# Kernel optimization log

Measured on AMD Instinct MI355X. Metric: run time of the kernel, lower is better.

The kernel has to match this reference:

```python
import jax, jax.numpy as jnp
import numpy as np

B, H, W, E = 4, 128, 128, 512
NH = 16
WH = WW = 8
DFF = 2048
EPS = 1e-5
N = WH * WW  # tokens per window
HD = E // NH  # head dim

# static relative-position index table: bias[q, k] = table[k_h - q_h + WH-1, k_w - q_w + WW-1]
_coords = np.stack(np.meshgrid(np.arange(WH), np.arange(WW), indexing='ij'), -1).reshape(-1, 2)  # (N, 2)
_rel = _coords[None, :, :] - _coords[:, None, :]  # (N, N, 2), key - query
_IDX_H = _rel[..., 0] + WH - 1
_IDX_W = _rel[..., 1] + WW - 1


def setup_inputs() -> dict:
    key = jax.random.key(0)
    ks = jax.random.split(key, 8)
    s = 0.02
    return {
        'x': jax.random.normal(ks[0], (B, H * W, E), jnp.float32),
        'in_proj_weight': jax.random.normal(ks[1], (3 * E, E), jnp.float32) * s,
        'in_proj_bias': jnp.zeros((3 * E,), jnp.float32),
        'out_proj_weight': jax.random.normal(ks[2], (E, E), jnp.float32) * s,
        'out_proj_bias': jnp.zeros((E,), jnp.float32),
        'pos_emb': jax.random.normal(ks[3], (2 * WH - 1, 2 * WW - 1, 1), jnp.float32) * s,
        'lin1_w': jax.random.normal(ks[4], (DFF, E), jnp.float32) * s,
        'lin1_b': jnp.zeros((DFF,), jnp.float32),
        'lin2_w': jax.random.normal(ks[5], (E, DFF), jnp.float32) * s,
        'lin2_b': jnp.zeros((E,), jnp.float32),
        'ln1_w': jnp.ones((E,), jnp.float32),
        'ln1_b': jnp.zeros((E,), jnp.float32),
        'ln2_w': jnp.ones((E,), jnp.float32),
        'ln2_b': jnp.zeros((E,), jnp.float32),
    }


def _layer_norm(y, g, b):
    m = y.mean(-1, keepdims=True)
    v = y.var(-1, keepdims=True)
    return (y - m) * jax.lax.rsqrt(v + EPS) * g + b


def _forward(x, in_proj_weight, in_proj_bias, out_proj_weight, out_proj_bias,
             pos_emb, lin1_w, lin1_b, lin2_w, lin2_b, ln1_w, ln1_b, ln2_w, ln2_b):
    # relative positional bias shared across heads: (1, N, N)
    bias = pos_emb[_IDX_H, _IDX_W, :].transpose(2, 0, 1)

    def attn(y):
        # window partition: (B, H*W, E) -> (B*nWin, N, E)
        yw = y.reshape(B, H // WH, WH, W // WW, WW, E)
        yw = yw.transpose(0, 1, 3, 2, 4, 5).reshape(-1, N, E)
        qw, kw, vw = jnp.split(in_proj_weight, 3, axis=0)
        qb, kb, vb = jnp.split(in_proj_bias, 3, axis=0)
        q = (yw @ qw.T + qb).reshape(-1, N, NH, HD).transpose(0, 2, 1, 3)  # (Bw, h, N, d)
        k = (yw @ kw.T + kb).reshape(-1, N, NH, HD).transpose(0, 2, 1, 3)
        v = (yw @ vw.T + vb).reshape(-1, N, NH, HD).transpose(0, 2, 1, 3)
        scores = jnp.einsum('bhqd,bhkd->bhqk', q, k) / np.sqrt(HD).astype(np.float32)
        scores = scores + bias[None]  # broadcast over windows and heads
        a = jax.nn.softmax(scores, axis=-1)
        o = jnp.einsum('bhqk,bhkd->bhqd', a, v)
        o = o.transpose(0, 2, 1, 3).reshape(-1, N, E)
        o = o @ out_proj_weight.T + out_proj_bias
        # reverse window partition
        o = o.reshape(B, H // WH, W // WW, WH, WW, E)
        return o.transpose(0, 1, 3, 2, 4, 5).reshape(B, H * W, E)

    # post-norm (norm_first=False): x = norm1(x + SA(x)); x = norm2(x + FF(x))
    z = _layer_norm(x + attn(x), ln1_w, ln1_b)
    ff = jax.nn.relu(z @ lin1_w.T + lin1_b) @ lin2_w.T + lin2_b
    return _layer_norm(z + ff, ln2_w, ln2_b)


def reference(x, in_proj_weight, in_proj_bias, out_proj_weight, out_proj_bias,
              pos_emb, lin1_w, lin1_b, lin2_w, lin2_b, ln1_w, ln1_b, ln2_w, ln2_b):
    return _forward(x, in_proj_weight, in_proj_bias, out_proj_weight, out_proj_bias,
                    pos_emb, lin1_w, lin1_b, lin2_w, lin2_b, ln1_w, ln1_b, ln2_w, ln2_b)
```

## Files before the change

### kernel.cpp

```cpp
#include <hip/hip_runtime.h>
#include <hip/hip_bf16.h>

#define NTOK   65536
#define E_     512
#define NH_    16
#define HD_    32
#define DFF_   2048
#define N3E    1536

typedef __attribute__((ext_vector_type(8))) short short8;
typedef __attribute__((ext_vector_type(4))) short short4t;
typedef __attribute__((ext_vector_type(4))) float floatx4;

__device__ inline float b2f(short u) {
    union { float f; unsigned int i; } x;
    x.i = ((unsigned int)(unsigned short)u) << 16;
    return x.f;
}
__device__ inline short f2bs(float f) {
    __hip_bfloat16 h = __float2bfloat16(f);
    return *reinterpret_cast<short*>(&h);
}

__global__ __launch_bounds__(256) void cvt_kernel(const float* __restrict__ in,
                                                  __hip_bfloat16* __restrict__ out, int n) {
    int i = (blockIdx.x * 256 + threadIdx.x) * 8;
    if (i >= n) return;
    if (i + 7 < n) {
        float4 a = *(const float4*)(in + i);
        float4 b = *(const float4*)(in + i + 4);
        short8 o;
        o[0] = f2bs(a.x); o[1] = f2bs(a.y); o[2] = f2bs(a.z); o[3] = f2bs(a.w);
        o[4] = f2bs(b.x); o[5] = f2bs(b.y); o[6] = f2bs(b.z); o[7] = f2bs(b.w);
        *(short8*)(out + i) = o;
    } else {
        for (int u = i; u < n; ++u) out[u] = __float2bfloat16(in[u]);
    }
}

template<int EPI>
__global__ __launch_bounds__(512) void gemm2_kernel(
    const __hip_bfloat16* __restrict__ A,
    const __hip_bfloat16* __restrict__ Bw,
    const float* __restrict__ bias,
    const void* __restrict__ res,
    void* __restrict__ out,
    int M, int N, int K)
{
    __shared__ __align__(16) short As[2][128 * 64];
    __shared__ __align__(16) short Bs[2][256 * 64];

    const int tid  = threadIdx.x;
    const int wid  = tid >> 6;
    const int lane = tid & 63;
    const int tileN = blockIdx.x * 256;
    const int tileM = blockIdx.y * 128;

    const int wm = (wid >> 2) * 64;
    const int wn = (wid & 3) * 64;
    const int lm = lane & 15;
    const int g  = lane >> 4;

    const int lr = lane >> 3;
    const int ss = (lane & 7) ^ lr;

    const __hip_bfloat16* gA = A  + (size_t)(tileM + wid * 16 + lr) * K + ss * 8;
    const __hip_bfloat16* gB = Bw + (size_t)(tileN + wid * 32 + lr) * K + ss * 8;

    floatx4 acc[4][4];
    #pragma unroll
    for (int i = 0; i < 4; ++i)
        #pragma unroll
        for (int j = 0; j < 4; ++j)
            acc[i][j] = (floatx4){0.f, 0.f, 0.f, 0.f};

#define STAGE2(b, k0)                                                                     \
    {                                                                                     \
        _Pragma("unroll")                                                                 \
        for (int q = 0; q < 2; ++q)                                                       \
            __builtin_amdgcn_global_load_lds(                                             \
                (const __attribute__((address_space(1))) void*)(gA + (size_t)(q * 8) * K + (k0)), \
                (__attribute__((address_space(3))) void*)(&As[b][(wid * 2 + q) * 512]),   \
                16, 0, 0);                                                                \
        _Pragma("unroll")                                                                 \
        for (int q = 0; q < 4; ++q)                                                       \
            __builtin_amdgcn_global_load_lds(                                             \
                (const __attribute__((address_space(1))) void*)(gB + (size_t)(q * 8) * K + (k0)), \
                (__attribute__((address_space(3))) void*)(&Bs[b][(wid * 4 + q) * 512]),   \
                16, 0, 0);                                                                \
    }

    const int NT = K >> 6;

    STAGE2(0, 0)
    STAGE2(1, 64)
    asm volatile("s_waitcnt vmcnt(6)\ns_barrier" ::: "memory");

    const int lsw = (lm & 7);

    for (int t = 0; t < NT; ++t) {
        const int b = t & 1;
        const short* pa = As[b];
        const short* pb = Bs[b];

        #pragma unroll
        for (int ks = 0; ks < 2; ++ks) {
            short8 af[4], bfr[4];
            const int cs = ks * 4 + g;
            const int so = (cs ^ lsw) * 8;
            #pragma unroll
            for (int i = 0; i < 4; ++i)
                af[i] = *(const short8*)(pa + (wm + i * 16 + lm) * 64 + so);
            #pragma unroll
            for (int j = 0; j < 4; ++j)
                bfr[j] = *(const short8*)(pb + (wn + j * 16 + lm) * 64 + so);

            __builtin_amdgcn_s_setprio(1);
            #pragma unroll
            for (int i = 0; i < 4; ++i)
                #pragma unroll
                for (int j = 0; j < 4; ++j)
                    acc[i][j] = __builtin_amdgcn_mfma_f32_16x16x32_bf16(af[i], bfr[j], acc[i][j], 0, 0, 0);
            __builtin_amdgcn_s_setprio(0);
        }

        if (t + 1 < NT) {
            asm volatile("s_waitcnt lgkmcnt(0)\ns_barrier" ::: "memory");
            if (t + 2 < NT) {
                STAGE2(b, (t + 2) * 64)
                asm volatile("s_waitcnt vmcnt(6)\ns_barrier" ::: "memory");
            } else {
                asm volatile("s_waitcnt vmcnt(0)\ns_barrier" ::: "memory");
            }
        }
    }
#undef STAGE2

    const int rbase = g * 4;
    #pragma unroll
    for (int i = 0; i < 4; ++i) {
        const int rl = wm + i * 16 + rbase;
        #pragma unroll
        for (int j = 0; j < 4; ++j) {
            const int n = tileN + wn + j * 16 + lm;
            const float bv = bias[n];
            #pragma unroll
            for (int r = 0; r < 4; ++r) {
                const int m = tileM + rl + r;
                const size_t idx = (size_t)m * N + n;
                float v = acc[i][j][r] + bv;
                if (EPI == 0) {
                    ((__hip_bfloat16*)out)[idx] = __float2bfloat16(v);
                } else if (EPI == 1) {
                    v += ((const float*)res)[idx];
                    ((float*)out)[idx] = v;
                } else if (EPI == 2) {
                    v = v > 0.f ? v : 0.f;
                    ((__hip_bfloat16*)out)[idx] = __float2bfloat16(v);
                } else {
                    v += __bfloat162float(((const __hip_bfloat16*)res)[idx]);
                    ((float*)out)[idx] = v;
                }
            }
        }
    }
}

__global__ __launch_bounds__(64) void attn_kernel(
    const __hip_bfloat16* __restrict__ qkv,
    const float* __restrict__ pos,
    __hip_bfloat16* __restrict__ obuf)
{
    __shared__ __align__(16) short vt[32][72];
    __shared__ __align__(16) short pl[64][72];
    __shared__ float ps[232];

    const int bwin = blockIdx.x;
    const int win  = bwin & 255;
    const int bat  = bwin >> 8;
    const int h    = blockIdx.y;
    const int l    = threadIdx.x;
    const int l15  = l & 15;
    const int g    = l >> 4;
    const int g8   = g * 8;

    const int base0 = bat * 16384 + (win >> 4) * 1024 + (win & 15) * 8;

    for (int u = l; u < 225; u += 64) ps[u] = pos[u];

    const int tok_l = base0 + (l >> 3) * 128 + (l & 7);
    const short8* vp = (const short8*)(qkv + (size_t)tok_l * N3E + 1024 + h * HD_);
    #pragma unroll
    for (int u = 0; u < 4; ++u) {
        short8 vv = vp[u];
        #pragma unroll
        for (int e = 0; e < 8; ++e) vt[u * 8 + e][l] = vv[e];
    }

    const int tokbase = base0 + (l15 >> 3) * 128 + (l15 & 7);
    short8 qf[4], kf[4];
    #pragma unroll
    for (int j = 0; j < 4; ++j) {
        const size_t tb = (size_t)(tokbase + 256 * j) * N3E + h * HD_ + g8;
        qf[j] = *(const short8*)(qkv + tb);
        kf[j] = *(const short8*)(qkv + tb + 512);
    }
    __syncthreads();

    floatx4 st[4][4];
    #pragma unroll
    for (int i = 0; i < 4; ++i)
        #pragma unroll
        for (int j = 0; j < 4; ++j)
            st[i][j] = __builtin_amdgcn_mfma_f32_16x16x32_bf16(
                kf[i], qf[j], (floatx4){0.f, 0.f, 0.f, 0.f}, 0, 0, 0);

    const float scale = 0.17677669529663687f;
    int kb[4];
    #pragma unroll
    for (int r = 0; r < 4; ++r) {
        const int qq = g * 4 + r;
        kb[r] = (qq >> 3) * 15 + (qq & 7);
    }

    #pragma unroll
    for (int j = 0; j < 4; ++j) {
        const int q   = j * 16 + l15;
        const int qoi = 112 - (q >> 3) * 15 - (q & 7);
        float p[16];
        float mx = -1e30f;
        #pragma unroll
        for (int i = 0; i < 4; ++i)
            #pragma unroll
            for (int r = 0; r < 4; ++r) {
                const float sv = st[i][j][r] * scale + ps[30 * i + kb[r] + qoi];
                p[i * 4 + r] = sv;
                mx = fmaxf(mx, sv);
            }
        mx = fmaxf(mx, __shfl_xor(mx, 16));
        mx = fmaxf(mx, __shfl_xor(mx, 32));
        float sum = 0.f;
        #pragma unroll
        for (int u = 0; u < 16; ++u) { p[u] = __expf(p[u] - mx); sum += p[u]; }
        sum += __shfl_xor(sum, 16);
        sum += __shfl_xor(sum, 32);
        const float inv = 1.f / sum;
        #pragma unroll
        for (int i = 0; i < 4; ++i) {
            short4t pk;
            #pragma unroll
            for (int r = 0; r < 4; ++r) pk[r] = f2bs(p[i * 4 + r] * inv);
            *(short4t*)&pl[q][i * 16 + g * 4] = pk;
        }
    }
    __syncthreads();

    short8 vb[2][2];
    #pragma unroll
    for (int nt = 0; nt < 2; ++nt)
        #pragma unroll
        for (int kk = 0; kk < 2; ++kk)
            vb[nt][kk] = *(const short8*)&vt[nt * 16 + l15][kk * 32 + g8];

    floatx4 o[4][2];
    #pragma unroll
    for (int j = 0; j < 4; ++j)
        #pragma unroll
        for (int nt = 0; nt < 2; ++nt)
            o[j][nt] = (floatx4){0.f, 0.f, 0.f, 0.f};

    #pragma unroll
    for (int j = 0; j < 4; ++j) {
        #pragma unroll
        for (int kk = 0; kk < 2; ++kk) {
            const short8 pa = *(const short8*)&pl[j * 16 + l15][kk * 32 + g8];
            #pragma unroll
            for (int nt = 0; nt < 2; ++nt)
                o[j][nt] = __builtin_amdgcn_mfma_f32_16x16x32_bf16(
                    pa, vb[nt][kk], o[j][nt], 0, 0, 0);
        }
    }

    #pragma unroll
    for (int r = 0; r < 4; ++r) {
        const int qq = g * 4 + r;
        const int tb = base0 + (qq >> 3) * 128 + (qq & 7);
        #pragma unroll
        for (int j = 0; j < 4; ++j) {
            __hip_bfloat16* op = obuf + (size_t)(tb + 256 * j) * E_ + h * HD_ + l15;
            op[0]  = __float2bfloat16(o[j][0][r]);
            op[16] = __float2bfloat16(o[j][1][r]);
        }
    }
}

template<int OUTMODE>
__global__ __launch_bounds__(256) void ln_kernel(
    const float* __restrict__ in, const float* __restrict__ gw,
    const float* __restrict__ gb, void* __restrict__ out)
{
    const int row  = blockIdx.x * 4 + (threadIdx.x >> 6);
    const int lane = threadIdx.x & 63;
    const float* rp = in + (size_t)row * 512 + lane * 8;
    float4 v0 = *(const float4*)rp;
    float4 v1 = *(const float4*)(rp + 4);
    float s  = v0.x + v0.y + v0.z + v0.w + v1.x + v1.y + v1.z + v1.w;
    float sq = v0.x * v0.x + v0.y * v0.y + v0.z * v0.z + v0.w * v0.w
             + v1.x * v1.x + v1.y * v1.y + v1.z * v1.z + v1.w * v1.w;
    #pragma unroll
    for (int off = 32; off > 0; off >>= 1) {
        s  += __shfl_xor(s, off);
        sq += __shfl_xor(sq, off);
    }
    const float mean = s * (1.f / 512.f);
    const float var  = sq * (1.f / 512.f) - mean * mean;
    const float rstd = rsqrtf(var + 1e-5f);
    const int c = lane * 8;
    float4 g0 = *(const float4*)(gw + c), g1 = *(const float4*)(gw + c + 4);
    float4 b0 = *(const float4*)(gb + c), b1 = *(const float4*)(gb + c + 4);
    float r[8];
    r[0] = (v0.x - mean) * rstd * g0.x + b0.x;
    r[1] = (v0.y - mean) * rstd * g0.y + b0.y;
    r[2] = (v0.z - mean) * rstd * g0.z + b0.z;
    r[3] = (v0.w - mean) * rstd * g0.w + b0.w;
    r[4] = (v1.x - mean) * rstd * g1.x + b1.x;
    r[5] = (v1.y - mean) * rstd * g1.y + b1.y;
    r[6] = (v1.z - mean) * rstd * g1.z + b1.z;
    r[7] = (v1.w - mean) * rstd * g1.w + b1.w;
    if (OUTMODE == 0) {
        short8 o;
        #pragma unroll
        for (int e = 0; e < 8; ++e) o[e] = f2bs(r[e]);
        *(short8*)((__hip_bfloat16*)out + (size_t)row * 512 + c) = o;
    } else {
        float* po = (float*)out + (size_t)row * 512 + c;
        *(float4*)po       = make_float4(r[0], r[1], r[2], r[3]);
        *(float4*)(po + 4) = make_float4(r[4], r[5], r[6], r[7]);
    }
}

static const size_t OFF_WQKV = 0;
static const size_t OFF_WOUT = 1572864;
static const size_t OFF_W1   = 2097152;
static const size_t OFF_W2   = 4194304;
static const size_t OFF_XB   = 6291456;
static const size_t OFF_ZB   = 73400320;
static const size_t OFF_QKVC = 140509184;
static const size_t OFF_OBUFC= 341835776;
static const size_t OFF_H1C  = OFF_QKVC;

extern "C" void kernel_launch(void* const* d_in, const int* in_sizes, int n_in,
                              void* d_out, int out_size, void* d_ws, size_t ws_size,
                              hipStream_t stream) {
    (void)in_sizes; (void)n_in; (void)out_size; (void)ws_size;
    const float* x    = (const float*)d_in[0];
    const float* wqkv = (const float*)d_in[1];
    const float* bqkv = (const float*)d_in[2];
    const float* wout = (const float*)d_in[3];
    const float* bout = (const float*)d_in[4];
    const float* pos  = (const float*)d_in[5];
    const float* w1   = (const float*)d_in[6];
    const float* b1   = (const float*)d_in[7];
    const float* w2   = (const float*)d_in[8];
    const float* b2   = (const float*)d_in[9];
    const float* g1   = (const float*)d_in[10];
    const float* bb1  = (const float*)d_in[11];
    const float* g2   = (const float*)d_in[12];
    const float* bb2  = (const float*)d_in[13];
    float* outp = (float*)d_out;

    char* ws = (char*)d_ws;
    __hip_bfloat16* wqkv_b = (__hip_bfloat16*)(ws + OFF_WQKV);
    __hip_bfloat16* wout_b = (__hip_bfloat16*)(ws + OFF_WOUT);
    __hip_bfloat16* w1_b   = (__hip_bfloat16*)(ws + OFF_W1);
    __hip_bfloat16* w2_b   = (__hip_bfloat16*)(ws + OFF_W2);
    __hip_bfloat16* xb     = (__hip_bfloat16*)(ws + OFF_XB);
    __hip_bfloat16* zb     = (__hip_bfloat16*)(ws + OFF_ZB);
    __hip_bfloat16* qkvc   = (__hip_bfloat16*)(ws + OFF_QKVC);
    __hip_bfloat16* obufc  = (__hip_bfloat16*)(ws + OFF_OBUFC);
    __hip_bfloat16* h1c    = (__hip_bfloat16*)(ws + OFF_H1C);

    {
        int n;
        n = N3E * E_;    cvt_kernel<<<(n / 8 + 255) / 256, 256, 0, stream>>>(wqkv, wqkv_b, n);
        n = E_ * E_;     cvt_kernel<<<(n / 8 + 255) / 256, 256, 0, stream>>>(wout, wout_b, n);
        n = DFF_ * E_;   cvt_kernel<<<(n / 8 + 255) / 256, 256, 0, stream>>>(w1, w1_b, n);
        n = E_ * DFF_;   cvt_kernel<<<(n / 8 + 255) / 256, 256, 0, stream>>>(w2, w2_b, n);
        n = NTOK * E_;   cvt_kernel<<<(n / 8 + 255) / 256, 256, 0, stream>>>(x, xb, n);
    }

    gemm2_kernel<0><<<dim3(N3E / 256, NTOK / 128), 512, 0, stream>>>(
        xb, wqkv_b, bqkv, nullptr, qkvc, NTOK, N3E, E_);
    attn_kernel<<<dim3(1024, NH_), 64, 0, stream>>>(qkvc, pos, obufc);
    gemm2_kernel<1><<<dim3(E_ / 256, NTOK / 128), 512, 0, stream>>>(
        obufc, wout_b, bout, x, outp, NTOK, E_, E_);

    ln_kernel<0><<<NTOK / 4, 256, 0, stream>>>(outp, g1, bb1, zb);

    gemm2_kernel<2><<<dim3(DFF_ / 256, NTOK / 128), 512, 0, stream>>>(
        zb, w1_b, b1, nullptr, h1c, NTOK, DFF_, E_);
    gemm2_kernel<3><<<dim3(E_ / 256, NTOK / 128), 512, 0, stream>>>(
        h1c, w2_b, b2, zb, outp, NTOK, E_, DFF_);

    ln_kernel<1><<<NTOK / 4, 256, 0, stream>>>(outp, g2, bb2, outp);
}
```

Baseline: 1.183 ms.

## Shrink GEMM tiles to 128x128x32 with 256 threads for higher occupancy

The GEMM kernel now uses a 128x128 output tile with K-step 32 and 4 waves of 256 threads, where it previously used a 128x256 tile with K-step 64 and 8 waves. The LDS swizzle and load mapping are rewritten for the 32-wide K rows, and launch bounds request 4 blocks per CU. The goal is to cut shared memory per block (32KB instead of 96KB) so more blocks stay resident and latency hides better. The cost is less data reuse per tile, twice as many barriers per K, and more global reads of A across N tiles.

```diff
diff --git a/kernel.cpp b/kernel.cpp
--- a/kernel.cpp
+++ b/kernel.cpp
@@ -39,7 +39,7 @@
 }
 
 template<int EPI>
-__global__ __launch_bounds__(512) void gemm2_kernel(
+__global__ __launch_bounds__(256, 4) void gemm3_kernel(
     const __hip_bfloat16* __restrict__ A,
     const __hip_bfloat16* __restrict__ Bw,
     const float* __restrict__ bias,
@@ -47,25 +47,25 @@
     void* __restrict__ out,
     int M, int N, int K)
 {
-    __shared__ __align__(16) short As[2][128 * 64];
-    __shared__ __align__(16) short Bs[2][256 * 64];
+    __shared__ __align__(16) short As[2][128 * 32];
+    __shared__ __align__(16) short Bs[2][128 * 32];
 
     const int tid  = threadIdx.x;
     const int wid  = tid >> 6;
     const int lane = tid & 63;
-    const int tileN = blockIdx.x * 256;
+    const int tileN = blockIdx.x * 128;
     const int tileM = blockIdx.y * 128;
 
-    const int wm = (wid >> 2) * 64;
-    const int wn = (wid & 3) * 64;
+    const int wm = (wid >> 1) * 64;
+    const int wn = (wid & 1) * 64;
     const int lm = lane & 15;
     const int g  = lane >> 4;
 
-    const int lr = lane >> 3;
-    const int ss = (lane & 7) ^ lr;
-
-    const __hip_bfloat16* gA = A  + (size_t)(tileM + wid * 16 + lr) * K + ss * 8;
-    const __hip_bfloat16* gB = Bw + (size_t)(tileN + wid * 32 + lr) * K + ss * 8;
+    const int lr = lane >> 2;
+    const int sl = (lane & 3) ^ (lr & 3);
+
+    const __hip_bfloat16* gA = A  + (size_t)(tileM + wid * 32 + lr) * K + sl * 8;
+    const __hip_bfloat16* gB = Bw + (size_t)(tileN + wid * 32 + lr) * K + sl * 8;
 
     floatx4 acc[4][4];
     #pragma unroll
@@ -74,67 +74,62 @@
         for (int j = 0; j < 4; ++j)
             acc[i][j] = (floatx4){0.f, 0.f, 0.f, 0.f};
 
-#define STAGE2(b, k0)                                                                     \
+#define STAGE3(b, k0)                                                                     \
     {                                                                                     \
         _Pragma("unroll")                                                                 \
         for (int q = 0; q < 2; ++q)                                                       \
             __builtin_amdgcn_global_load_lds(                                             \
-                (const __attribute__((address_space(1))) void*)(gA + (size_t)(q * 8) * K + (k0)), \
+                (const __attribute__((address_space(1))) void*)(gA + (size_t)(q * 16) * K + (k0)), \
                 (__attribute__((address_space(3))) void*)(&As[b][(wid * 2 + q) * 512]),   \
                 16, 0, 0);                                                                \
         _Pragma("unroll")                                                                 \
-        for (int q = 0; q < 4; ++q)                                                       \
+        for (int q = 0; q < 2; ++q)                                                       \
             __builtin_amdgcn_global_load_lds(                                             \
-                (const __attribute__((address_space(1))) void*)(gB + (size_t)(q * 8) * K + (k0)), \
-                (__attribute__((address_space(3))) void*)(&Bs[b][(wid * 4 + q) * 512]),   \
+                (const __attribute__((address_space(1))) void*)(gB + (size_t)(q * 16) * K + (k0)), \
+                (__attribute__((address_space(3))) void*)(&Bs[b][(wid * 2 + q) * 512]),   \
                 16, 0, 0);                                                                \
     }
 
-    const int NT = K >> 6;
-
-    STAGE2(0, 0)
-    STAGE2(1, 64)
-    asm volatile("s_waitcnt vmcnt(6)\ns_barrier" ::: "memory");
-
-    const int lsw = (lm & 7);
+    const int NT = K >> 5;
+
+    STAGE3(0, 0)
+    STAGE3(1, 32)
+    asm volatile("s_waitcnt vmcnt(4)\ns_barrier" ::: "memory");
+
+    const int so = (g ^ (lm & 3)) * 8;
 
     for (int t = 0; t < NT; ++t) {
         const int b = t & 1;
         const short* pa = As[b];
         const short* pb = Bs[b];
 
-        #pragma unroll
-        for (int ks = 0; ks < 2; ++ks) {
-            short8 af[4], bfr[4];
-            const int cs = ks * 4 + g;
-            const int so = (cs ^ lsw) * 8;
-            #pragma unroll
-            for (int i = 0; i < 4; ++i)
-                af[i] = *(const short8*)(pa + (wm + i * 16 + lm) * 64 + so);
+        short8 af[4], bfr[4];
+        #pragma unroll
+        for (int i = 0; i < 4; ++i)
+            af[i] = *(const short8*)(pa + (wm + i * 16 + lm) * 32 + so);
+        #pragma unroll
+        for (int j = 0; j < 4; ++j)
+            bfr[j] = *(const short8*)(pb + (wn + j * 16 + lm) * 32 + so);
+
+        __builtin_amdgcn_s_setprio(1);
+        #pragma unroll
+        for (int i = 0; i < 4; ++i)
             #pragma unroll
             for (int j = 0; j < 4; ++j)
-                bfr[j] = *(const short8*)(pb + (wn + j * 16 + lm) * 64 + so);
-
-            __builtin_amdgcn_s_setprio(1);
-            #pragma unroll
-            for (int i = 0; i < 4; ++i)
-                #pragma unroll
-                for (int j = 0; j < 4; ++j)
-                    acc[i][j] = __builtin_amdgcn_mfma_f32_16x16x32_bf16(af[i], bfr[j], acc[i][j], 0, 0, 0);
-            __builtin_amdgcn_s_setprio(0);
-        }
+                acc[i][j] = __builtin_amdgcn_mfma_f32_16x16x32_bf16(af[i], bfr[j], acc[i][j], 0, 0, 0);
+        __builtin_amdgcn_s_setprio(0);
 
         if (t + 1 < NT) {
             asm volatile("s_waitcnt lgkmcnt(0)\ns_barrier" ::: "memory");
             if (t + 2 < NT) {
-                STAGE2(b, (t + 2) * 64)
-                asm volatile("s_waitcnt vmcnt(6)\ns_barrier" ::: "memory");
+                STAGE3(b, (t + 2) * 32)
+                asm volatile("s_waitcnt vmcnt(4)\ns_barrier" ::: "memory");
             } else {
                 asm volatile("s_waitcnt vmcnt(0)\ns_barrier" ::: "memory");
             }
         }
     }
-#undef STAGE2
+#undef STAGE3
 
     const int rbase = g * 4;
     #pragma unroll
@@ -389,17 +384,17 @@
         n = NTOK * E_;   cvt_kernel<<<(n / 8 + 255) / 256, 256, 0, stream>>>(x, xb, n);
     }
 
-    gemm2_kernel<0><<<dim3(N3E / 256, NTOK / 128), 512, 0, stream>>>(
+    gemm3_kernel<0><<<dim3(N3E / 128, NTOK / 128), 256, 0, stream>>>(
         xb, wqkv_b, bqkv, nullptr, qkvc, NTOK, N3E, E_);
     attn_kernel<<<dim3(1024, NH_), 64, 0, stream>>>(qkvc, pos, obufc);
-    gemm2_kernel<1><<<dim3(E_ / 256, NTOK / 128), 512, 0, stream>>>(
+    gemm3_kernel<1><<<dim3(E_ / 128, NTOK / 128), 256, 0, stream>>>(
         obufc, wout_b, bout, x, outp, NTOK, E_, E_);
 
     ln_kernel<0><<<NTOK / 4, 256, 0, stream>>>(outp, g1, bb1, zb);
 
-    gemm2_kernel<2><<<dim3(DFF_ / 256, NTOK / 128), 512, 0, stream>>>(
+    gemm3_kernel<2><<<dim3(DFF_ / 128, NTOK / 128), 256, 0, stream>>>(
         zb, w1_b, b1, nullptr, h1c, NTOK, DFF_, E_);
-    gemm2_kernel<3><<<dim3(E_ / 256, NTOK / 128), 512, 0, stream>>>(
+    gemm3_kernel<3><<<dim3(E_ / 128, NTOK / 128), 256, 0, stream>>>(
         h1c, w2_b, b2, zb, outp, NTOK, E_, DFF_);
 
     ln_kernel<1><<<NTOK / 4, 256, 0, stream>>>(outp, g2, bb2, outp);
```

Result: faster. 1.074 ms (-9.2%).
